# Kernel optimization log

Measured on AMD Instinct MI355X. Metric: run time of the kernel, lower is better.

## Reference

```python
import jax, jax.numpy as jnp
import numpy as np

N_HEAD = 8
D_HEAD = 64
HIDDEN = 512
T = 2048
BS = 4
SCALE = D_HEAD ** -0.5


def setup_inputs() -> dict:
    key = jax.random.key(0)
    k1, k2, k3 = jax.random.split(key, 3)
    x = jax.random.normal(k1, (BS, T, HIDDEN), dtype=jnp.float32)
    # torch Linear weight is (out,in); we store as (in,out) for x @ W
    W_qkv = jax.random.normal(k2, (HIDDEN, (2 * N_HEAD + 1) * D_HEAD), dtype=jnp.float32) * 0.02
    W_out = jax.random.normal(k3, (D_HEAD, HIDDEN), dtype=jnp.float32) * 0.02
    return {"x": x, "W_qkv": W_qkv, "W_out": W_out}


def reference(x, W_qkv, W_out):
    bs, t, h = x.shape
    qkv = x @ W_qkv  # (bs, t, (2H+1)*d)
    q, k, v = jnp.split(qkv, [N_HEAD * D_HEAD, 2 * N_HEAD * D_HEAD], axis=-1)
    q = q.reshape(bs, t, N_HEAD, D_HEAD)
    k = k.reshape(bs, t, N_HEAD, D_HEAD)
    # v is shared across heads: (bs, t, d)
    score = jnp.einsum("bqhd,bkhd->bhqk", q, k) * SCALE
    causal = jnp.triu(jnp.full((t, t), -jnp.inf, dtype=score.dtype), 1)
    score = score + causal[None, None, :, :]
    prob = jax.nn.softmax(score, axis=-1)  # (bs, H, t, t)
    attn_vec = jnp.einsum("bhqk,bkd->bhqd", prob, v)  # shared V broadcast over heads
    m_attn_vec = jnp.mean(attn_vec, axis=1)  # head-mean: (bs, t, d)
    out = m_attn_vec @ W_out  # (bs, t, hidden)
    return out, attn_vec
```

## Files before the change

### kernel.cpp

```cpp
#include <hip/hip_runtime.h>
#include <hip/hip_bf16.h>

#define NHEAD  8
#define DHEAD  64
#define HIDDEN 512
#define SEQ_T  2048
#define BATCH  4
#define NQKV   1088
#define QPITCH 1152
#define NT     32
#define NROWS  (BATCH * SEQ_T)
#define NBH    (BATCH * NHEAD)
#define QSC    (0.125f * 1.44269504f)

typedef __attribute__((ext_vector_type(8))) short short8;
typedef __attribute__((ext_vector_type(4))) float f32x4;

__device__ __forceinline__ unsigned short f2bf(float f) {
  unsigned int u = __float_as_uint(f);
  u += 0x7FFFu + ((u >> 16) & 1u);
  return (unsigned short)(u >> 16);
}
__device__ __forceinline__ float bf2f(unsigned short u) {
  return __uint_as_float((unsigned int)u << 16);
}

__device__ __forceinline__ void load_lds16(const unsigned short* g, unsigned short* l) {
  __builtin_amdgcn_global_load_lds((const __attribute__((address_space(1))) void*)g,
                                   (__attribute__((address_space(3))) void*)l, 16, 0, 0);
}

#define DPPF(x, ctrl) \
  __int_as_float(__builtin_amdgcn_update_dpp(0, __float_as_int(x), (ctrl), 0xF, 0xF, true))
__device__ __forceinline__ float rsum16(float x) {
  x += DPPF(x, 0xB1);
  x += DPPF(x, 0x4E);
  x += DPPF(x, 0x141);
  x += DPPF(x, 0x140);
  return x;
}

__global__ __launch_bounds__(256) void prep(const float* __restrict__ x,
                                            const float* __restrict__ W,
                                            unsigned short* __restrict__ xb,
                                            unsigned short* __restrict__ Wt) {
  const int bx = blockIdx.x;
  const int tid = threadIdx.x;
  if (bx < 2048) {
    const size_t i0 = ((size_t)bx * 256 + tid) * 8;
    float4 a = *(const float4*)(x + i0);
    float4 b = *(const float4*)(x + i0 + 4);
    ushort4 u0, u1;
    u0.x = f2bf(a.x); u0.y = f2bf(a.y); u0.z = f2bf(a.z); u0.w = f2bf(a.w);
    u1.x = f2bf(b.x); u1.y = f2bf(b.y); u1.z = f2bf(b.z); u1.w = f2bf(b.w);
    *(ushort4*)(xb + i0) = u0;
    *(ushort4*)(xb + i0 + 4) = u1;
    return;
  }
  if (bx >= 2184) {
    const int z = bx - 2184;
    const size_t base = (size_t)NQKV * HIDDEN + ((size_t)z * 256 + tid) * 16;
    uint4 zero = {0u, 0u, 0u, 0u};
    *(uint4*)(Wt + base) = zero;
    *(uint4*)(Wt + base + 8) = zero;
    return;
  }
  const int idx = bx - 2048;
  const int n0 = (idx % 17) * 64;
  const int k0 = (idx / 17) * 64;
  __shared__ float T[64 * 65];
#pragma unroll
  for (int i = 0; i < 4; ++i) {
    int f = tid + i * 256;
    int r = f >> 4;
    int c4 = (f & 15) * 4;
    float4 v = *(const float4*)(W + (size_t)(k0 + r) * NQKV + n0 + c4);
    T[r * 65 + c4 + 0] = v.x;
    T[r * 65 + c4 + 1] = v.y;
    T[r * 65 + c4 + 2] = v.z;
    T[r * 65 + c4 + 3] = v.w;
  }
  __syncthreads();
#pragma unroll
  for (int i = 0; i < 4; ++i) {
    int f = tid + i * 256;
    int n = f >> 4;
    int k4 = (f & 15) * 4;
    ushort4 u;
    u.x = f2bf(T[(k4 + 0) * 65 + n]);
    u.y = f2bf(T[(k4 + 1) * 65 + n]);
    u.z = f2bf(T[(k4 + 2) * 65 + n]);
    u.w = f2bf(T[(k4 + 3) * 65 + n]);
    *(ushort4*)(Wt + (size_t)(n0 + n) * HIDDEN + k0 + k4) = u;
  }
}

__global__ __launch_bounds__(256, 3) void qkv_mfma(const unsigned short* __restrict__ Xb,
                                                   const unsigned short* __restrict__ Wt,
                                                   unsigned short* __restrict__ Y) {
  __shared__ __align__(16) unsigned short As[128 * 64];
  __shared__ __align__(16) unsigned short Bs[128 * 64];
  const int L = blockIdx.x;
  const int slot = L >> 3;
  const int bm = (L & 7) * 8 + (slot & 7);
  const int bn = slot >> 3;
  const int tid = threadIdx.x;
  const int wave = tid >> 6;
  const int lane = tid & 63;
  const int quad = lane >> 4;
  const int l15 = lane & 15;
  const int lrow = lane >> 3;
  const int lchunk = lane & 7;

  const unsigned short* xrow = Xb + (size_t)bm * 128 * HIDDEN;
  const unsigned short* wrow = Wt + (size_t)bn * 128 * HIDDEN;

  f32x4 acc[2][8];
#pragma unroll
  for (int mt = 0; mt < 2; ++mt)
#pragma unroll
    for (int nt = 0; nt < 8; ++nt) acc[mt][nt] = (f32x4){0.f, 0.f, 0.f, 0.f};

  for (int k0 = 0; k0 < HIDDEN; k0 += 64) {
    __syncthreads();
#pragma unroll
    for (int c = 0; c < 4; ++c) {
      int call = wave * 4 + c;
      int m = call * 8 + lrow;
      int clog = lchunk ^ lrow;
      load_lds16(xrow + (size_t)m * HIDDEN + k0 + clog * 8, &As[call * 512]);
      load_lds16(wrow + (size_t)m * HIDDEN + k0 + clog * 8, &Bs[call * 512]);
    }
    __syncthreads();

#pragma unroll
    for (int ks = 0; ks < 2; ++ks) {
      short8 a[2], b[8];
#pragma unroll
      for (int mt = 0; mt < 2; ++mt) {
        int m = wave * 32 + mt * 16 + l15;
        int phys = (ks * 4 + quad) ^ (l15 & 7);
        a[mt] = *(const short8*)&As[m * 64 + phys * 8];
      }
#pragma unroll
      for (int nt = 0; nt < 8; ++nt) {
        int n = nt * 16 + l15;
        int phys = (ks * 4 + quad) ^ (l15 & 7);
        b[nt] = *(const short8*)&Bs[n * 64 + phys * 8];
      }
#pragma unroll
      for (int mt = 0; mt < 2; ++mt)
#pragma unroll
        for (int nt = 0; nt < 8; ++nt)
          acc[mt][nt] = __builtin_amdgcn_mfma_f32_16x16x32_bf16(a[mt], b[nt], acc[mt][nt], 0, 0, 0);
    }
  }

  const float qs = (bn < 4) ? QSC : 1.0f;
#pragma unroll
  for (int mt = 0; mt < 2; ++mt)
#pragma unroll
    for (int r = 0; r < 4; ++r) {
      int row = bm * 128 + wave * 32 + mt * 16 + quad * 4 + r;
#pragma unroll
      for (int nt = 0; nt < 8; ++nt) {
        int col = bn * 128 + nt * 16 + l15;
        Y[(size_t)row * QPITCH + col] = f2bf(acc[mt][nt][r] * qs);
      }
    }
}

__global__ __launch_bounds__(256) void v_transpose(const unsigned short* __restrict__ qkv,
                                                   unsigned short* __restrict__ vt) {
  const int b = blockIdx.x >> 5;
  const int k0 = (blockIdx.x & 31) * 64;
  const int tid = threadIdx.x;
  __shared__ unsigned short Vs[64 * 66];

#pragma unroll
  for (int i = 0; i < 8; ++i) {
    int c = tid + i * 256;
    int row = c >> 5;
    int col2 = c & 31;
    unsigned int v = *(const unsigned int*)(qkv + (size_t)(b * SEQ_T + k0 + row) * QPITCH + 1024 + col2 * 2);
    *(unsigned int*)&Vs[row * 66 + col2 * 2] = v;
  }
  __syncthreads();

#pragma unroll
  for (int i = 0; i < 16; ++i) {
    int f = tid + i * 256;
    int d = f >> 6;
    int n = f & 63;
    int c = ((n & 3) << 4) | (n >> 2);
    vt[((size_t)b * DHEAD + d) * SEQ_T + k0 + n] = Vs[c * 66 + d];
  }
}

__global__ __launch_bounds__(256, 3) void attn_pass(const unsigned short* __restrict__ qkv,
                                                    const unsigned short* __restrict__ vt,
                                                    unsigned short* __restrict__ pbuf0,
                                                    unsigned short* __restrict__ pbuf1,
                                                    float* __restrict__ lbuf) {
  const int bh = blockIdx.x;
  const int y = blockIdx.y;
  const int qt = 15 - (y >> 1);
  const int kh = y & 1;
  const int b = bh >> 3;
  const int h = bh & 7;
  const int tid = threadIdx.x;
  const int wave = tid >> 6;
  const int lane = tid & 63;
  const int quad = lane >> 4;
  const int l15 = lane & 15;

  __shared__ __align__(16) unsigned short Ks[2][64 * 64];
  __shared__ __align__(16) unsigned short Vts[2][64 * 64];
  __shared__ __align__(16) unsigned short Ps[128 * 72];

  const unsigned short* bq = qkv + (size_t)b * SEQ_T * QPITCH;
  const unsigned short* bvt = vt + (size_t)b * DHEAD * SEQ_T;

  const int q0 = qt * 128;
  const int kbeg = kh ? (qt + 1) : 0;
  const int kend = kh ? (2 * qt + 1) : qt;

  short8 aq[2][2];
#pragma unroll
  for (int s = 0; s < 2; ++s) {
    const unsigned short* qp = bq + (size_t)(q0 + s * 64 + wave * 16 + l15) * QPITCH + h * 64 + quad * 8;
    aq[s][0] = *(const short8*)qp;
    aq[s][1] = *(const short8*)(qp + 32);
  }

  f32x4 o[2][4];
#pragma unroll
  for (int s = 0; s < 2; ++s)
#pragma unroll
    for (int t = 0; t < 4; ++t) o[s][t] = (f32x4){0.f, 0.f, 0.f, 0.f};
  float l_part[2][4] = {{0.f, 0.f, 0.f, 0.f}, {0.f, 0.f, 0.f, 0.f}};

  const int srow = tid >> 3;
  const int sch = (tid & 7) ^ (srow & 7);
  const int ph0 = (quad ^ (l15 & 7)) * 8;

#pragma unroll
  for (int c = 0; c < 2; ++c) {
    load_lds16(bq + (size_t)(kbeg * 64 + c * 32 + srow) * QPITCH + 512 + h * 64 + sch * 8,
               &Ks[0][c * 2048 + wave * 512]);
    load_lds16(bvt + (size_t)(c * 32 + srow) * SEQ_T + kbeg * 64 + sch * 8,
               &Vts[0][c * 2048 + wave * 512]);
  }

  for (int kt = kbeg; kt <= kend; ++kt) {
    const int k0 = kt * 64;
    const int cur = (kt - kbeg) & 1;
    __syncthreads();
    if (kt < kend) {
      const int kn = (kt + 1) * 64;
      const int nxt = cur ^ 1;
#pragma unroll
      for (int c = 0; c < 2; ++c) {
        load_lds16(bq + (size_t)(kn + c * 32 + srow) * QPITCH + 512 + h * 64 + sch * 8,
                   &Ks[nxt][c * 2048 + wave * 512]);
        load_lds16(bvt + (size_t)(c * 32 + srow) * SEQ_T + kn + sch * 8,
                   &Vts[nxt][c * 2048 + wave * 512]);
      }
    }

    const unsigned short* ksb = Ks[cur];
    const unsigned short* vsb = Vts[cur];
    const bool needMask = (k0 + 63) > q0;

    short8 bk[4][2];
#pragma unroll
    for (int t = 0; t < 4; ++t) {
      const unsigned short* kp = &ksb[(l15 + 16 * t) * 64];
      bk[t][0] = *(const short8*)(kp + ph0);
      bk[t][1] = *(const short8*)(kp + (ph0 ^ 32));
    }

#pragma unroll
    for (int s = 0; s < 2; ++s) {
      f32x4 pr[4];
#pragma unroll
      for (int t = 0; t < 4; ++t) {
        f32x4 sv = (f32x4){0.f, 0.f, 0.f, 0.f};
        sv = __builtin_amdgcn_mfma_f32_16x16x32_bf16(aq[s][0], bk[t][0], sv, 0, 0, 0);
        sv = __builtin_amdgcn_mfma_f32_16x16x32_bf16(aq[s][1], bk[t][1], sv, 0, 0, 0);
        pr[t] = sv;
      }
      const int rbase = s * 64 + wave * 16 + quad * 4;
#pragma unroll
      for (int t = 0; t < 4; ++t)
#pragma unroll
        for (int r = 0; r < 4; ++r) {
          float p = __builtin_amdgcn_exp2f(pr[t][r]);
          if (needMask)
            p = (k0 + 16 * t + l15 <= q0 + rbase + r) ? p : 0.f;
          l_part[s][r] += p;
          pr[t][r] = p;
        }
#pragma unroll
      for (int r = 0; r < 4; ++r) {
        uint2 w;
        w.x = __builtin_amdgcn_perm(__float_as_uint(pr[1][r]), __float_as_uint(pr[0][r]), 0x07060302u);
        w.y = __builtin_amdgcn_perm(__float_as_uint(pr[3][r]), __float_as_uint(pr[2][r]), 0x07060302u);
        *(uint2*)&Ps[(rbase + r) * 72 + 4 * l15] = w;
      }
    }

    short8 bv[4][2];
#pragma unroll
    for (int t = 0; t < 4; ++t) {
      const unsigned short* vp = &vsb[(l15 + 16 * t) * 64];
      bv[t][0] = *(const short8*)(vp + ph0);
      bv[t][1] = *(const short8*)(vp + (ph0 ^ 32));
    }
    short8 ap[2][2];
#pragma unroll
    for (int s = 0; s < 2; ++s) {
      const unsigned short* pp = &Ps[(s * 64 + wave * 16 + l15) * 72];
      ap[s][0] = *(const short8*)(pp + quad * 8);
      ap[s][1] = *(const short8*)(pp + 32 + quad * 8);
    }

#pragma unroll
    for (int t = 0; t < 4; ++t)
#pragma unroll
      for (int s = 0; s < 2; ++s) {
        o[s][t] = __builtin_amdgcn_mfma_f32_16x16x32_bf16(ap[s][0], bv[t][0], o[s][t], 0, 0, 0);
        o[s][t] = __builtin_amdgcn_mfma_f32_16x16x32_bf16(ap[s][1], bv[t][1], o[s][t], 0, 0, 0);
      }
  }

  unsigned short* pb = kh ? pbuf1 : pbuf0;
#pragma unroll
  for (int s = 0; s < 2; ++s) {
#pragma unroll
    for (int r = 0; r < 4; ++r) {
      float l = rsum16(l_part[s][r]);
      const int trow = q0 + s * 64 + wave * 16 + quad * 4 + r;
      if (l15 == 0) lbuf[kh * (NBH * SEQ_T) + bh * SEQ_T + trow] = l;
      const size_t base = ((size_t)bh * SEQ_T + trow) * DHEAD;
#pragma unroll
      for (int t = 0; t < 4; ++t) pb[base + l15 + 16 * t] = f2bf(o[s][t][r]);
    }
  }
}

__global__ __launch_bounds__(256) void out_merge(const unsigned short* __restrict__ pbuf0,
                                                 const unsigned short* __restrict__ pbuf1,
                                                 const float* __restrict__ lbuf,
                                                 const float* __restrict__ Wout,
                                                 float* __restrict__ attnv,
                                                 float* __restrict__ out) {
  const int row0 = blockIdx.x * 16;
  const int tid = threadIdx.x;
  __shared__ float Ms[16][64];

  {
    const int lr = tid >> 4;
    const int d0 = (tid & 15) * 4;
    const int row = row0 + lr;
    const int b = row >> 11;
    const int t = row & 2047;
    float s0 = 0.f, s1 = 0.f, s2 = 0.f, s3 = 0.f;
#pragma unroll
    for (int hh = 0; hh < NHEAD; ++hh) {
      const size_t ridx = (size_t)(b * NHEAD + hh) * SEQ_T + t;
      const float inv = 1.0f / (lbuf[ridx] + lbuf[NBH * SEQ_T + ridx]);
      const size_t idx = ridx * DHEAD + d0;
      ushort4 A = *(const ushort4*)(pbuf0 + idx);
      ushort4 B = *(const ushort4*)(pbuf1 + idx);
      float4 m;
      m.x = (bf2f(A.x) + bf2f(B.x)) * inv;
      m.y = (bf2f(A.y) + bf2f(B.y)) * inv;
      m.z = (bf2f(A.z) + bf2f(B.z)) * inv;
      m.w = (bf2f(A.w) + bf2f(B.w)) * inv;
      *(float4*)(attnv + idx) = m;
      s0 += m.x; s1 += m.y; s2 += m.z; s3 += m.w;
    }
    Ms[lr][d0 + 0] = s0 * 0.125f;
    Ms[lr][d0 + 1] = s1 * 0.125f;
    Ms[lr][d0 + 2] = s2 * 0.125f;
    Ms[lr][d0 + 3] = s3 * 0.125f;
  }
  __syncthreads();

  const int c0 = tid * 2;
  float a0[16], a1[16];
#pragma unroll
  for (int i = 0; i < 16; ++i) { a0[i] = 0.f; a1[i] = 0.f; }

  for (int d = 0; d < 64; ++d) {
    float2 w = *(const float2*)(Wout + (size_t)d * HIDDEN + c0);
#pragma unroll
    for (int lr = 0; lr < 16; ++lr) {
      float m = Ms[lr][d];
      a0[lr] += m * w.x;
      a1[lr] += m * w.y;
    }
  }
#pragma unroll
  for (int lr = 0; lr < 16; ++lr) {
    float2 v = make_float2(a0[lr], a1[lr]);
    *(float2*)(out + (size_t)(row0 + lr) * HIDDEN + c0) = v;
  }
}

extern "C" void kernel_launch(void* const* d_in, const int* in_sizes, int n_in,
                              void* d_out, int out_size, void* d_ws, size_t ws_size,
                              hipStream_t stream) {
  const float* x     = (const float*)d_in[0];
  const float* W_qkv = (const float*)d_in[1];
  const float* W_out = (const float*)d_in[2];

  float* out      = (float*)d_out;
  float* attn_vec = out + (size_t)BATCH * SEQ_T * HIDDEN;

  unsigned short* qkv  = (unsigned short*)d_ws;
  unsigned short* vt   = qkv + (size_t)NROWS * QPITCH;
  unsigned short* xb   = vt + (size_t)BATCH * DHEAD * SEQ_T;
  unsigned short* Wt   = xb + (size_t)NROWS * HIDDEN;
  unsigned short* pbuf0 = Wt + (size_t)QPITCH * HIDDEN;
  unsigned short* pbuf1 = pbuf0 + (size_t)NBH * SEQ_T * DHEAD;
  float*          lbuf  = (float*)(pbuf1 + (size_t)NBH * SEQ_T * DHEAD);

  prep<<<dim3(2048 + 136 + 8), 256, 0, stream>>>(x, W_qkv, xb, Wt);
  qkv_mfma<<<dim3(576), 256, 0, stream>>>(xb, Wt, qkv);
  v_transpose<<<dim3(BATCH * NT), 256, 0, stream>>>(qkv, vt);
  attn_pass<<<dim3(NBH, 32), 256, 0, stream>>>(qkv, vt, pbuf0, pbuf1, lbuf);
  out_merge<<<dim3(512), 256, 0, stream>>>(pbuf0, pbuf1, lbuf, W_out, attn_vec, out);
}
```

Before: 143.0 us.

## Keep P in registers by transposing S=K·Qᵀ and permuting V layout

Swaps the MFMA operands so each lane holds scores for one query row across consecutive keys. The exp'd probabilities can then be packed straight into the A-operand registers for the PV MFMA, which removes the Ps shared-memory round trip. The V-transpose prep kernel permutes the key ordering to match the new register layout. Row sums are now a per-lane accumulation reduced with two shuffles at the end, and freeing Ps LDS lets launch bounds target 4 blocks per SM instead of 3. This depends on the key permutation in vt exactly matching the MFMA register ordering.

Measured after the change: 142.9 us. About the same (-0.1%).

```diff
diff --git a/kernel.cpp b/kernel.cpp
--- a/kernel.cpp
+++ b/kernel.cpp
@@ -28,16 +28,6 @@
 __device__ __forceinline__ void load_lds16(const unsigned short* g, unsigned short* l) {
   __builtin_amdgcn_global_load_lds((const __attribute__((address_space(1))) void*)g,
                                    (__attribute__((address_space(3))) void*)l, 16, 0, 0);
-}
-
-#define DPPF(x, ctrl) \
-  __int_as_float(__builtin_amdgcn_update_dpp(0, __float_as_int(x), (ctrl), 0xF, 0xF, true))
-__device__ __forceinline__ float rsum16(float x) {
-  x += DPPF(x, 0xB1);
-  x += DPPF(x, 0x4E);
-  x += DPPF(x, 0x141);
-  x += DPPF(x, 0x140);
-  return x;
 }
 
 __global__ __launch_bounds__(256) void prep(const float* __restrict__ x,
@@ -192,12 +182,12 @@
     int f = tid + i * 256;
     int d = f >> 6;
     int n = f & 63;
-    int c = ((n & 3) << 4) | (n >> 2);
+    int c = (n & 32) | ((n & 4) << 2) | ((n >> 1) & 12) | (n & 3);
     vt[((size_t)b * DHEAD + d) * SEQ_T + k0 + n] = Vs[c * 66 + d];
   }
 }
 
-__global__ __launch_bounds__(256, 3) void attn_pass(const unsigned short* __restrict__ qkv,
+__global__ __launch_bounds__(256, 4) void attn_pass(const unsigned short* __restrict__ qkv,
                                                     const unsigned short* __restrict__ vt,
                                                     unsigned short* __restrict__ pbuf0,
                                                     unsigned short* __restrict__ pbuf1,
@@ -216,7 +206,6 @@
 
   __shared__ __align__(16) unsigned short Ks[2][64 * 64];
   __shared__ __align__(16) unsigned short Vts[2][64 * 64];
-  __shared__ __align__(16) unsigned short Ps[128 * 72];
 
   const unsigned short* bq = qkv + (size_t)b * SEQ_T * QPITCH;
   const unsigned short* bvt = vt + (size_t)b * DHEAD * SEQ_T;
@@ -238,7 +227,7 @@
   for (int s = 0; s < 2; ++s)
 #pragma unroll
     for (int t = 0; t < 4; ++t) o[s][t] = (f32x4){0.f, 0.f, 0.f, 0.f};
-  float l_part[2][4] = {{0.f, 0.f, 0.f, 0.f}, {0.f, 0.f, 0.f, 0.f}};
+  float l_part[2] = {0.f, 0.f};
 
   const int srow = tid >> 3;
   const int sch = (tid & 7) ^ (srow & 7);
@@ -280,33 +269,40 @@
       bk[t][1] = *(const short8*)(kp + (ph0 ^ 32));
     }
 
+    short8 ap[2][2];
 #pragma unroll
     for (int s = 0; s < 2; ++s) {
       f32x4 pr[4];
 #pragma unroll
       for (int t = 0; t < 4; ++t) {
         f32x4 sv = (f32x4){0.f, 0.f, 0.f, 0.f};
-        sv = __builtin_amdgcn_mfma_f32_16x16x32_bf16(aq[s][0], bk[t][0], sv, 0, 0, 0);
-        sv = __builtin_amdgcn_mfma_f32_16x16x32_bf16(aq[s][1], bk[t][1], sv, 0, 0, 0);
+        sv = __builtin_amdgcn_mfma_f32_16x16x32_bf16(bk[t][0], aq[s][0], sv, 0, 0, 0);
+        sv = __builtin_amdgcn_mfma_f32_16x16x32_bf16(bk[t][1], aq[s][1], sv, 0, 0, 0);
         pr[t] = sv;
       }
-      const int rbase = s * 64 + wave * 16 + quad * 4;
+      const int qrow = q0 + s * 64 + wave * 16 + l15;
 #pragma unroll
       for (int t = 0; t < 4; ++t)
 #pragma unroll
         for (int r = 0; r < 4; ++r) {
           float p = __builtin_amdgcn_exp2f(pr[t][r]);
           if (needMask)
-            p = (k0 + 16 * t + l15 <= q0 + rbase + r) ? p : 0.f;
-          l_part[s][r] += p;
+            p = (k0 + 16 * t + 4 * quad + r <= qrow) ? p : 0.f;
+          l_part[s] += p;
           pr[t][r] = p;
         }
 #pragma unroll
-      for (int r = 0; r < 4; ++r) {
-        uint2 w;
-        w.x = __builtin_amdgcn_perm(__float_as_uint(pr[1][r]), __float_as_uint(pr[0][r]), 0x07060302u);
-        w.y = __builtin_amdgcn_perm(__float_as_uint(pr[3][r]), __float_as_uint(pr[2][r]), 0x07060302u);
-        *(uint2*)&Ps[(rbase + r) * 72 + 4 * l15] = w;
+      for (int c = 0; c < 2; ++c) {
+        union { unsigned int u[4]; short8 v; } pk;
+        pk.u[0] = __builtin_amdgcn_perm(__float_as_uint(pr[2 * c][1]),
+                                        __float_as_uint(pr[2 * c][0]), 0x07060302u);
+        pk.u[1] = __builtin_amdgcn_perm(__float_as_uint(pr[2 * c][3]),
+                                        __float_as_uint(pr[2 * c][2]), 0x07060302u);
+        pk.u[2] = __builtin_amdgcn_perm(__float_as_uint(pr[2 * c + 1][1]),
+                                        __float_as_uint(pr[2 * c + 1][0]), 0x07060302u);
+        pk.u[3] = __builtin_amdgcn_perm(__float_as_uint(pr[2 * c + 1][3]),
+                                        __float_as_uint(pr[2 * c + 1][2]), 0x07060302u);
+        ap[s][c] = pk.v;
       }
     }
 
@@ -317,13 +313,6 @@
       bv[t][0] = *(const short8*)(vp + ph0);
       bv[t][1] = *(const short8*)(vp + (ph0 ^ 32));
     }
-    short8 ap[2][2];
-#pragma unroll
-    for (int s = 0; s < 2; ++s) {
-      const unsigned short* pp = &Ps[(s * 64 + wave * 16 + l15) * 72];
-      ap[s][0] = *(const short8*)(pp + quad * 8);
-      ap[s][1] = *(const short8*)(pp + 32 + quad * 8);
-    }
 
 #pragma unroll
     for (int t = 0; t < 4; ++t)
@@ -337,11 +326,14 @@
   unsigned short* pb = kh ? pbuf1 : pbuf0;
 #pragma unroll
   for (int s = 0; s < 2; ++s) {
+    float l = l_part[s];
+    l += __shfl_xor(l, 16);
+    l += __shfl_xor(l, 32);
+    if (lane < 16)
+      lbuf[kh * (NBH * SEQ_T) + bh * SEQ_T + q0 + s * 64 + wave * 16 + l15] = l;
 #pragma unroll
     for (int r = 0; r < 4; ++r) {
-      float l = rsum16(l_part[s][r]);
       const int trow = q0 + s * 64 + wave * 16 + quad * 4 + r;
-      if (l15 == 0) lbuf[kh * (NBH * SEQ_T) + bh * SEQ_T + trow] = l;
       const size_t base = ((size_t)bh * SEQ_T + trow) * DHEAD;
 #pragma unroll
       for (int t = 0; t < 4; ++t) pb[base + l15 + 16 * t] = f2bf(o[s][t][r]);
```
